# Optimization experiments

Measured on AMD Instinct MI355X. Metric: run time of the kernel, lower is better.

The kernel has to match this reference:

```python
import jax, jax.numpy as jnp
import numpy as np

# BatchNorm1d in eval mode with default init (gamma=1, beta=0, mean=0, var=1):
# y = x / sqrt(1 + eps)
BN_S = 1.0 / float(np.sqrt(1.0 + 1e-5))
ROI_THRESH = 0.8
DN = ('NCHW', 'OIHW', 'NCHW')


def conv(x, w, stride=1, pad=1):
    return jax.lax.conv_general_dilated(x, w, (stride, stride), ((pad, pad), (pad, pad)), dimension_numbers=DN)


def inv_conv(x, w):
    # dense equivalent of spconv.SparseInverseConv2d paired with a stride-2, pad-1, k=3 conv:
    # adjoint index map = transposed conv (lhs_dilation=2, flipped kernel, pad (1,2))
    return jax.lax.conv_general_dilated(x, jnp.flip(w, (2, 3)), (1, 1), ((1, 2), (1, 2)), lhs_dilation=(2, 2), dimension_numbers=DN)


def downsample_mask(m):
    # active-site generation rule of a stride-2, pad-1, k=3 sparse conv == 3x3/stride-2 max pool
    return jax.lax.reduce_window(m, 0.0, jax.lax.max, (1, 1, 3, 3), (1, 1, 2, 2), ((0, 0), (0, 0), (1, 1), (1, 1)))


def setup_inputs():
    key = jax.random.key(0)
    ks = jax.random.split(key, 24)
    b, n_i, H, W = 2, 4, 384, 384
    s = 0.1  # weight scale to keep activations bounded through the conv stack
    inp = {
        'x': jax.random.normal(ks[0], (b, 64, H // 4, W // 4), jnp.float32),
        'image': jax.random.normal(ks[1], (b, 3, H, W), jnp.float32),
        'masks': jax.random.uniform(ks[2], (b, n_i, H, W), jnp.float32),
        'roi_masks': jax.random.uniform(ks[3], (b, n_i, H, W), jnp.float32),
        'w1a': jax.random.normal(ks[4], (32, 4, 3, 3), jnp.float32) * s,
        'w1b': jax.random.normal(ks[5], (32, 32, 3, 3), jnp.float32) * s,
        'w2a': jax.random.normal(ks[6], (32, 32, 3, 3), jnp.float32) * s,
        'w2b': jax.random.normal(ks[7], (32, 32, 3, 3), jnp.float32) * s,
        'w4a': jax.random.normal(ks[8], (64, 32, 3, 3), jnp.float32) * s,
        'w4b': jax.random.normal(ks[9], (64, 64, 3, 3), jnp.float32) * s,
        'inv4_w': jax.random.normal(ks[10], (64, 64, 3, 3), jnp.float32) * s,
        'l4_sub_w': jax.random.normal(ks[11], (32, 64, 3, 3), jnp.float32) * s,
        'inv2_w': jax.random.normal(ks[12], (32, 32, 3, 3), jnp.float32) * s,
        'l5_sub_w': jax.random.normal(ks[13], (32, 32, 3, 3), jnp.float32) * s,
        'r4_w1': jax.random.normal(ks[14], (32, 64, 3, 3), jnp.float32) * s,
        'r4_w2': jax.random.normal(ks[15], (1, 32, 3, 3), jnp.float32) * s,
        'r4_b2': jax.random.normal(ks[16], (1,), jnp.float32) * s,
        'r1_w1': jax.random.normal(ks[17], (32, 32, 3, 3), jnp.float32) * s,
        'r1_w2': jax.random.normal(ks[18], (1, 32, 3, 3), jnp.float32) * s,
        'r1_b2': jax.random.normal(ks[19], (1,), jnp.float32) * s,
    }
    return inp


def reference(x, image, masks, roi_masks, w1a, w1b, w2a, w2b, w4a, w4b, inv4_w, l4_sub_w, inv2_w, l5_sub_w, r4_w1, r4_w2, r4_b2, r1_w1, r1_w2, r1_b2):
    # Faithful dense emulation of predict_details: SubMConv == conv(masked x)*mask,
    # stride-2 SparseConv == conv(masked x) masked by max-pooled mask,
    # SparseInverseConv == transposed conv masked by parent-resolution mask,
    # Fsp.sparse_add on shared indices == masked add, dense()-99/+99 == where(mask, v, -99).
    b, n_i, H, W = masks.shape
    N = b * n_i
    m = masks.reshape(N, 1, H, W)
    roi = roi_masks.reshape(N, 1, H, W)
    img = jnp.broadcast_to(image[:, None], (b, n_i, 3, H, W)).reshape(N, 3, H, W)
    inp = jnp.concatenate([img, m], axis=1)  # [N,4,H,W]

    mask1 = (roi > ROI_THRESH).astype(inp.dtype)
    mask2 = downsample_mask(mask1)
    mask4 = downsample_mask(mask2)

    # low_os1_module: SubMConv, ReLU, BN, SubMConv, ReLU, BN
    f = jnp.maximum(conv(inp * mask1, w1a) * mask1, 0.0) * BN_S
    fea1 = jnp.maximum(conv(f, w1b) * mask1, 0.0) * BN_S  # [N,32,H,W]
    # low_os2_module: stride-2 SparseConv, ReLU, BN, SubMConv, ReLU, BN
    g = jnp.maximum(conv(fea1, w2a, stride=2) * mask2, 0.0) * BN_S
    fea2 = jnp.maximum(conv(g, w2b) * mask2, 0.0) * BN_S  # [N,32,H/2,W/2]
    # low_os4_module
    h = jnp.maximum(conv(fea2, w4a, stride=2) * mask4, 0.0) * BN_S
    fea3 = jnp.maximum(conv(h, w4b) * mask4, 0.0) * BN_S  # [N,64,H/4,W/4]

    # gather dense OS4 features at sparse sites (batch index // n_i) + sparse_add
    xg = jnp.broadcast_to(x[:, None], (b, n_i) + x.shape[1:]).reshape(N, *x.shape[1:]) * mask4
    xs = xg + fea3

    # refine_OS4: SubMConv, BN, leaky, SubMConv(+bias); dense() with -99 off-support
    t = jax.nn.leaky_relu(conv(xs, r4_w1) * mask4 * BN_S, 0.2)
    t = (conv(t, r4_w2) + r4_b2[None, :, None, None]) * mask4
    x_os4_out = jnp.where(mask4 > 0, t, -99.0)

    # layer4: SparseInverseConv(64->64) to OS2 sites, BN, leaky, SubMConv(64->32); add fea2
    u = jax.nn.leaky_relu(inv_conv(xs, inv4_w) * mask2 * BN_S, 0.2)
    u = conv(u, l4_sub_w) * mask2 + fea2
    # layer5: SparseInverseConv(32->32) to OS1 sites, BN, leaky, SubMConv(32->32); add fea1
    v = jax.nn.leaky_relu(inv_conv(u, inv2_w) * mask1 * BN_S, 0.2)
    v = conv(v, l5_sub_w) * mask1 + fea1

    # refine_OS1
    t1 = jax.nn.leaky_relu(conv(v, r1_w1) * mask1 * BN_S, 0.2)
    t1 = (conv(t1, r1_w2) + r1_b2[None, :, None, None]) * mask1
    x_os1_out = jnp.where(mask1 > 0, t1, -99.0)
    return x_os4_out, x_os1_out
```

## Files before the change

### kernel.cpp

```cpp
#include <hip/hip_runtime.h>
#include <hip/hip_bf16.h>

using bf16 = __hip_bfloat16;
typedef unsigned char u8;
typedef short bf16x8 __attribute__((ext_vector_type(8)));
typedef short bf16x4 __attribute__((ext_vector_type(4)));
typedef float f32x4 __attribute__((ext_vector_type(4)));

#define BNS 0.9999950000374997f
#define MFMA_B16 __builtin_amdgcn_mfma_f32_16x16x32_bf16

__device__ __forceinline__ short f2bs(float v){ bf16 h = __float2bfloat16(v); return *reinterpret_cast<short*>(&h); }
__device__ __forceinline__ float s2f(short s){ union{unsigned u; float f;} x; x.u = ((unsigned)(unsigned short)s) << 16; return x.f; }
__device__ __forceinline__ float lrelu(float a){ return fmaxf(a, 0.2f*a); }
__device__ __forceinline__ bf16x8 ld8(const short* p){ return *(const bf16x8*)(p); }


__global__ __launch_bounds__(256) void k_mask1(const float* __restrict__ roi, u8* __restrict__ m1, int total){
    int i = blockIdx.x*256 + threadIdx.x;
    if (i < total) m1[i] = (roi[i] > 0.8f) ? 1 : 0;
}

__global__ __launch_bounds__(256) void k_down(const u8* __restrict__ mi, u8* __restrict__ mo,
                                              int IH, int IW, int OH, int OW){
    int p = blockIdx.x*256 + threadIdx.x;
    int n = blockIdx.y;
    if (p >= OH*OW) return;
    int oy = p / OW, ox = p - oy*OW;
    const u8* src = mi + (size_t)n*IH*IW;
    int v = 0;
    #pragma unroll
    for (int ky=0; ky<3; ky++){
        int iy = 2*oy + ky - 1;
        if ((unsigned)iy >= (unsigned)IH) continue;
        #pragma unroll
        for (int kx=0; kx<3; kx++){
            int ix = 2*ox + kx - 1;
            if ((unsigned)ix < (unsigned)IW) v |= src[iy*IW + ix];
        }
    }
    mo[(size_t)n*OH*OW + p] = (u8)v;
}

__global__ __launch_bounds__(256) void k_wprep(const float* __restrict__ w1b,
                                               const float* __restrict__ i2,
                                               const float* __restrict__ l5,
                                               const float* __restrict__ r1a,
                                               const float* __restrict__ w2b,
                                               const float* __restrict__ w2a,
                                               short* __restrict__ dst){
    int a = blockIdx.y;
    const float* src = (a==0)? w1b : (a==1)? i2 : (a==2)? l5 : (a==3)? r1a : (a==4)? w2b : w2a;
    float sc = (a==2) ? 1.0f : BNS;
    int j = blockIdx.x*256 + threadIdx.x;
    if (j < 9216){
        int co = j/288, r = j%288, ci = r/9, k = r%9;
        dst[a*9216 + k*1024 + co*32 + ci] = f2bs(src[j]*sc);
    }
}

__global__ __launch_bounds__(256) void k_wprep4(const float* __restrict__ inv4,
                                                const float* __restrict__ w4b,
                                                const float* __restrict__ l4s,
                                                const float* __restrict__ r4w1,
                                                const float* __restrict__ w4a,
                                                short* __restrict__ dst)
{
    int a = blockIdx.y;
    int j = blockIdx.x*256 + threadIdx.x;
    if (a < 2){
        if (j < 36864){
            int co = j/576, r = j%576, ci = r/9, k = r%9;
            const float* s = a ? w4b : inv4;
            dst[a*36864 + k*4096 + co*64 + ci] = f2bs(s[j]*BNS);
        }
    } else if (a < 4){
        if (j < 18432){
            int co = j/576, r = j%576, ci = r/9, k = r%9;
            const float* s = (a==2) ? l4s : r4w1;
            float sc = (a==2) ? 1.0f : BNS;
            dst[73728 + (a-2)*18432 + k*2048 + co*64 + ci] = f2bs(s[j]*sc);
        }
    } else {
        if (j < 18432){
            int co = j/288, r = j%288, ci = r/9, k = r%9;
            dst[110592 + k*2048 + co*32 + ci] = f2bs(w4a[j]*BNS);
        }
    }
}

__global__ __launch_bounds__(256) void k_wprep_misc(const float* __restrict__ w1a,
                                                    const float* __restrict__ r1w2,
                                                    const float* __restrict__ r4w2,
                                                    short* __restrict__ d1a,
                                                    short* __restrict__ dh){
    int a = blockIdx.y;
    int j = blockIdx.x*256 + threadIdx.x;
    if (a == 0){
        if (j < 2048){
            int h = j >> 10, r = j & 1023, co = r >> 5, kq = r & 31;
            int q = h*32 + kq;
            d1a[j] = (q < 36) ? f2bs(w1a[co*36 + q]*BNS) : 0;
        }
    } else {
        if (j < 4608){
            int k = j/512, r = j%512, co = r/32, ci = r%32;
            const float* s = (a==1) ? r1w2 : r4w2;
            dh[(a-1)*4608 + j] = (co == 0) ? f2bs(s[ci*9 + k]) : 0;
        }
    }
}

template<int CIN, int COUT, int EPI, int TH>
__global__ __launch_bounds__(256) void mconv_s1(const short* __restrict__ in, int H,
                                                const short* __restrict__ wT,
                                                const u8* __restrict__ mask,
                                                const float* __restrict__ res32,
                                                short* __restrict__ out, int tilesX)
{
    const int HW = H*H;
    const int HV = CIN/32, G = COUT/16, CH8 = CIN/8;
    const int SR = TH + 2;
    const int SITES = SR*18;
    const int PS = (SITES | 1)*8;
    const int U2N = TH/4;
    int tY = blockIdx.x / tilesX, tX = blockIdx.x % tilesX, n = blockIdx.z;
    int y0 = tY*TH, x0 = tX*16;

    __shared__ __align__(16) short s_in[CH8*((SITES|1)*8)];
    __shared__ u8 s_m[TH*16];

    int tid = threadIdx.x;
    const short* inN = in + (size_t)n*HW*CIN;
    for (int i = tid; i < SITES*CH8; i += 256){
        int r = i/CH8, q = i%CH8;
        int ry = r/18, rx = r%18;
        int gy = y0-1+ry, gx = x0-1+rx;
        bf16x8 v = {0,0,0,0,0,0,0,0};
        if ((unsigned)gy < (unsigned)H && (unsigned)gx < (unsigned)H)
            v = *(const bf16x8*)(inN + ((size_t)gy*H + gx)*CIN + q*8);
        *(bf16x8*)(s_in + q*PS + r*8) = v;
    }
    for (int i = tid; i < TH*16; i += 256){
        int ty = i>>4, tx = i&15;
        s_m[i] = mask[(size_t)n*HW + (y0+ty)*H + x0+tx];
    }
    __syncthreads();

    int wv = tid >> 6, lane = tid & 63;
    int nQ = lane >> 4, nn = lane & 15;

    f32x4 acc[U2N][G];
    #pragma unroll
    for (int u2=0; u2<U2N; ++u2)
        #pragma unroll
        for (int g=0; g<G; ++g) acc[u2][g] = (f32x4){0,0,0,0};

    #pragma unroll
    for (int h=0; h<HV; ++h){
        const short* bh[U2N];
        #pragma unroll
        for (int u2=0; u2<U2N; ++u2){
            int ty = u2*4 + wv;
            bh[u2] = s_in + (h*4+nQ)*PS + (ty*18 + nn)*8;
        }
        #pragma unroll
        for (int ky=0; ky<3; ++ky)
            #pragma unroll
            for (int kx=0; kx<3; ++kx){
                const int k = ky*3+kx;
                bf16x8 a[G];
                #pragma unroll
                for (int g=0; g<G; ++g)
                    a[g] = *(const bf16x8*)(wT + k*COUT*CIN + (g*16+nn)*CIN + h*32 + nQ*8);
                #pragma unroll
                for (int u2=0; u2<U2N; ++u2){
                    bf16x8 bfr = ld8(bh[u2] + (ky*18+kx)*8);
                    #pragma unroll
                    for (int g=0; g<G; ++g)
                        acc[u2][g] = MFMA_B16(a[g], bfr, acc[u2][g], 0,0,0);
                }
            }
    }

    #pragma unroll
    for (int u2=0; u2<U2N; ++u2){
        int nt = u2*4 + wv;
        int p = (y0+nt)*H + x0+nn;
        u8 m = s_m[nt*16 + nn];
        short* op = out + ((size_t)n*HW + p)*COUT;
        #pragma unroll
        for (int g=0; g<G; ++g){
            float r[4];
            #pragma unroll
            for (int e=0; e<4; ++e){
                int co = g*16 + nQ*4 + e;
                float a = acc[u2][g][e], o;
                if      (EPI == 0) o = m ? fmaxf(a,0.f) : 0.f;
                else if (EPI == 1) o = m ? lrelu(a) : 0.f;
                else o = m ? fmaxf(a,0.f) + res32[((size_t)(n>>2)*COUT + co)*(size_t)HW + p] : 0.f;
                r[e] = o;
            }
            bf16x4 w4 = {f2bs(r[0]),f2bs(r[1]),f2bs(r[2]),f2bs(r[3])};
            *(bf16x4*)(op + g*16 + nQ*4) = w4;
        }
    }
}

template<int TH>
__global__ __launch_bounds__(256) void mconv_head32(const short* __restrict__ in, int H,
                                                    const short* __restrict__ wTh,
                                                    const float* __restrict__ bias,
                                                    const u8* __restrict__ mask,
                                                    float* __restrict__ out, int tilesX)
{
    const int HW = H*H;
    const int SR = TH + 2, SITES = SR*18;
    const int PS = (SITES|1)*8;
    int tY = blockIdx.x / tilesX, tX = blockIdx.x % tilesX, n = blockIdx.z;
    int y0 = tY*TH, x0 = tX*16;

    __shared__ __align__(16) short s_in[4*((SITES|1)*8)];
    __shared__ u8 s_m[TH*16];

    int tid = threadIdx.x;
    const short* inN = in + (size_t)n*HW*32;
    for (int i = tid; i < SITES*4; i += 256){
        int r = i>>2, q = i&3;
        int ry = r/18, rx = r%18;
        int gy = y0-1+ry, gx = x0-1+rx;
        bf16x8 v = {0,0,0,0,0,0,0,0};
        if ((unsigned)gy < (unsigned)H && (unsigned)gx < (unsigned)H)
            v = *(const bf16x8*)(inN + ((size_t)gy*H + gx)*32 + q*8);
        *(bf16x8*)(s_in + q*PS + r*8) = v;
    }
    for (int i = tid; i < TH*16; i += 256){
        int ty = i>>4, tx = i&15;
        s_m[i] = mask[(size_t)n*HW + (y0+ty)*H + x0+tx];
    }
    __syncthreads();

    int wv = tid >> 6, lane = tid & 63;
    int nQ = lane >> 4, nn = lane & 15;
    float bb = bias[0];

    for (int nt = wv; nt < TH; nt += 4){
        const short* bp = s_in + nQ*PS + (nt*18 + nn)*8;
        f32x4 acc = {0,0,0,0};
        #pragma unroll
        for (int ky=0; ky<3; ++ky)
            #pragma unroll
            for (int kx=0; kx<3; ++kx){
                const int k = ky*3+kx;
                bf16x8 aw = *(const bf16x8*)(wTh + k*512 + nn*32 + nQ*8);
                bf16x8 bfr = ld8(bp + (ky*18+kx)*8);
                acc = MFMA_B16(aw, bfr, acc, 0,0,0);
            }
        if (nQ == 0){
            u8 m = s_m[nt*16 + nn];
            int p = (y0+nt)*H + x0+nn;
            out[(size_t)n*HW + p] = m ? acc[0] + bb : -99.f;
        }
    }
}

template<int COUT, int THO>
__global__ __launch_bounds__(256) void mconv_s2m(const short* __restrict__ in, int IH,
                                                 const short* __restrict__ wT,
                                                 const u8* __restrict__ mask,
                                                 short* __restrict__ out, int OH, int tilesX)
{
    const int IHW = IH*IH, OHW = OH*OH, G = COUT/16;
    const int IR = 2*THO + 1;
    const int SITES = IR*33;
    const int PS = (SITES|1)*8;
    const int ITN = THO/4;
    int tY = blockIdx.x / tilesX, tX = blockIdx.x % tilesX, n = blockIdx.z;
    int y0 = tY*THO, x0 = tX*16;

    __shared__ __align__(16) short s_in[4*((SITES|1)*8)];
    __shared__ u8 s_m[THO*16];

    int tid = threadIdx.x;
    const short* inN = in + (size_t)n*IHW*32;
    for (int i = tid; i < SITES*4; i += 256){
        int r = i>>2, q = i&3;
        int ry = r/33, rx = r%33;
        int gy = 2*y0-1+ry, gx = 2*x0-1+rx;
        bf16x8 v = {0,0,0,0,0,0,0,0};
        if ((unsigned)gy < (unsigned)IH && (unsigned)gx < (unsigned)IH)
            v = *(const bf16x8*)(inN + ((size_t)gy*IH + gx)*32 + q*8);
        *(bf16x8*)(s_in + q*PS + r*8) = v;
    }
    for (int i = tid; i < THO*16; i += 256){
        int ty = i>>4, tx = i&15;
        s_m[i] = mask[(size_t)n*OHW + (y0+ty)*OH + x0+tx];
    }
    __syncthreads();

    int wv = tid >> 6, lane = tid & 63;
    int nQ = lane >> 4, nn = lane & 15;

    f32x4 acc[ITN][G];
    #pragma unroll
    for (int it=0; it<ITN; ++it)
        #pragma unroll
        for (int g=0; g<G; ++g) acc[it][g] = (f32x4){0,0,0,0};

    const short* pb[ITN];
    #pragma unroll
    for (int it=0; it<ITN; ++it){
        int nt = it*4 + wv;
        pb[it] = s_in + nQ*PS + ((2*nt)*33 + 2*nn)*8;
    }

    #pragma unroll
    for (int ky=0; ky<3; ++ky)
        #pragma unroll
        for (int kx=0; kx<3; ++kx){
            const int k = ky*3+kx;
            bf16x8 a[G];
            #pragma unroll
            for (int g=0; g<G; ++g)
                a[g] = *(const bf16x8*)(wT + k*COUT*32 + (g*16+nn)*32 + nQ*8);
            #pragma unroll
            for (int it=0; it<ITN; ++it){
                bf16x8 bfr = ld8(pb[it] + (ky*33+kx)*8);
                #pragma unroll
                for (int g=0; g<G; ++g)
                    acc[it][g] = MFMA_B16(a[g], bfr, acc[it][g], 0,0,0);
            }
        }

    #pragma unroll
    for (int it=0; it<ITN; ++it){
        int nt = it*4 + wv;
        int p = (y0+nt)*OH + x0+nn;
        u8 m = s_m[nt*16 + nn];
        short* op = out + ((size_t)n*OHW + p)*COUT;
        #pragma unroll
        for (int g=0; g<G; ++g){
            float r[4];
            #pragma unroll
            for (int e=0; e<4; ++e) r[e] = m ? fmaxf(acc[it][g][e],0.f) : 0.f;
            bf16x4 w4 = {f2bs(r[0]),f2bs(r[1]),f2bs(r[2]),f2bs(r[3])};
            *(bf16x4*)(op + g*16 + nQ*4) = w4;
        }
    }
}

__global__ __launch_bounds__(256) void conv1ab3(const float* __restrict__ image,
                                                const float* __restrict__ masks,
                                                const u8*  __restrict__ M1,
                                                const short* __restrict__ wT1a,
                                                const short* __restrict__ wT1b,
                                                short* __restrict__ fea1)
{
    const int H = 384; const int HW = H*H;
    const int PS = 181*8;
    int tY = blockIdx.x / 48, tX = blockIdx.x % 48, n = blockIdx.z;
    int y0 = tY*16, x0 = tX*8;

    __shared__ float s_inp[4][240];
    __shared__ u8    s_m[240];
    __shared__ __align__(16) short s_ic[8*(181*8)];
    short* s_f = s_ic;

    int tid = threadIdx.x;
    for (int i = tid; i < 240; i += 256){
        int ly = i/12, lxx = i%12;
        int gy = y0-2+ly, gx = x0-2+lxx;
        bool inb = ((unsigned)gy < 384u) && ((unsigned)gx < 384u);
        u8 mv = inb ? M1[(size_t)n*HW + gy*H + gx] : 0;
        s_m[i] = mv;
        float mm = (float)mv;
        int p = gy*H + gx;
        #pragma unroll
        for (int c = 0; c < 4; ++c){
            float v = 0.f;
            if (inb) v = (c < 3) ? image[((size_t)(n>>2)*3 + c)*HW + p]
                                 : masks[(size_t)n*HW + p];
            s_inp[c][i] = v*mm;
        }
    }
    __syncthreads();

    for (int i = tid; i < 180*64; i += 256){
        int site = i >> 6, q = i & 63;
        short v = 0;
        if (q < 36){
            int ci = q/9, k = q - ci*9, ky = k/3, kx = k - ky*3;
            int fy = site/10, fx = site - fy*10;
            v = f2bs(s_inp[ci][(fy+ky)*12 + fx+kx]);
        }
        s_ic[(q>>3)*PS + site*8 + (q&7)] = v;
    }
    __syncthreads();

    int wv = tid >> 6, lane = tid & 63;
    int nQ = lane >> 4, nn = lane & 15;

    f32x4 fr[3][2];
    {
        #pragma unroll
        for (int u=0; u<3; ++u){ fr[u][0] = (f32x4){0,0,0,0}; fr[u][1] = (f32x4){0,0,0,0}; }
        #pragma unroll
        for (int h=0; h<2; ++h){
            bf16x8 fa0 = *(const bf16x8*)(wT1a + h*1024 + nn*32 + nQ*8);
            bf16x8 fa1 = *(const bf16x8*)(wT1a + h*1024 + (16+nn)*32 + nQ*8);
            #pragma unroll
            for (int u=0; u<3; ++u){
                int nt = u*4 + wv;
                int s0 = nt*16 + nn;
                int s = s0 > 179 ? 179 : s0;
                bf16x8 bfr = ld8(s_ic + (h*4+nQ)*PS + s*8);
                fr[u][0] = MFMA_B16(fa0, bfr, fr[u][0], 0,0,0);
                fr[u][1] = MFMA_B16(fa1, bfr, fr[u][1], 0,0,0);
            }
        }
    }
    __syncthreads();

    #pragma unroll
    for (int u=0; u<3; ++u){
        int nt = u*4 + wv;
        int s0 = nt*16 + nn;
        if (s0 <= 179){
            int fy = s0/10, fx = s0 - fy*10;
            u8 m = s_m[(fy+1)*12 + fx+1];
            #pragma unroll
            for (int g=0; g<2; ++g){
                float r[4];
                #pragma unroll
                for (int e=0; e<4; ++e){
                    float a = fr[u][g][e];
                    r[e] = m ? fmaxf(a,0.f) : 0.f;
                }
                bf16x4 w4 = {f2bs(r[0]),f2bs(r[1]),f2bs(r[2]),f2bs(r[3])};
                *(bf16x4*)(s_f + (g*2 + (nQ>>1))*PS + s0*8 + (nQ&1)*4) = w4;
            }
        }
    }
    __syncthreads();

    {
        f32x4 acc0[2], acc1[2];
        const short* pb[2];
        #pragma unroll
        for (int it=0; it<2; ++it){
            acc0[it] = (f32x4){0,0,0,0}; acc1[it] = (f32x4){0,0,0,0};
            int s0 = (it*4 + wv)*16 + nn;
            int ty = s0 >> 3, tx = s0 & 7;
            pb[it] = s_f + nQ*PS + (ty*10 + tx)*8;
        }
        #pragma unroll
        for (int ky=0; ky<3; ++ky)
            #pragma unroll
            for (int kx=0; kx<3; ++kx){
                const int k = ky*3+kx;
                bf16x8 a0 = *(const bf16x8*)(wT1b + k*1024 + nn*32 + nQ*8);
                bf16x8 a1 = *(const bf16x8*)(wT1b + k*1024 + (16+nn)*32 + nQ*8);
                #pragma unroll
                for (int it=0; it<2; ++it){
                    bf16x8 bfr = ld8(pb[it] + (ky*10+kx)*8);
                    acc0[it] = MFMA_B16(a0, bfr, acc0[it], 0,0,0);
                    acc1[it] = MFMA_B16(a1, bfr, acc1[it], 0,0,0);
                }
            }
        #pragma unroll
        for (int it=0; it<2; ++it){
            int s0 = (it*4 + wv)*16 + nn;
            int ty = s0 >> 3, tx = s0 & 7;
            u8 m = s_m[(ty+2)*12 + tx+2];
            short* fp = fea1 + ((size_t)n*HW + (size_t)(y0+ty)*H + (x0+tx))*32;
            #pragma unroll
            for (int g=0; g<2; ++g){
                float r[4];
                #pragma unroll
                for (int e=0; e<4; ++e){
                    float a = g ? acc1[it][e] : acc0[it][e];
                    r[e] = m ? fmaxf(a,0.f) : 0.f;
                }
                bf16x4 w4 = {f2bs(r[0]),f2bs(r[1]),f2bs(r[2]),f2bs(r[3])};
                *(bf16x4*)(fp + g*16 + nQ*4) = w4;
            }
        }
    }
}

__global__ __launch_bounds__(256) void fk_l4c(const short* __restrict__ xs,
                                              const short* __restrict__ fea2,
                                              const u8*  __restrict__ M2,
                                              const short* __restrict__ wTi4,
                                              const short* __restrict__ wTl4,
                                              short* __restrict__ u_out)
{
    const int H2 = 192, HW2 = H2*H2, H4 = 96, HW4 = H4*H4;
    const int PSX = 101*8, PSU = 325*8;
    int tY = blockIdx.x / 12, tX = blockIdx.x % 12, n = blockIdx.z;
    int y0 = tY*16, x0 = tX*16;
    int uy0 = (y0>>1) - 1, ux0 = (x0>>1) - 1;

    __shared__ __align__(16) short s_xs[8*(101*8)];
    __shared__ __align__(16) short s_ul[8*(325*8)];
    __shared__ u8 s_m[324];

    int tid = threadIdx.x;
    const short* xN = xs + (size_t)n*HW4*64;
    for (int i = tid; i < 100*8; i += 256){
        int r = i>>3, q = i&7;
        int ly = r/10, lxx = r%10;
        int gy = uy0+ly, gx = ux0+lxx;
        bf16x8 v = {0,0,0,0,0,0,0,0};
        if ((unsigned)gy < 96u && (unsigned)gx < 96u)
            v = *(const bf16x8*)(xN + ((size_t)gy*H4 + gx)*64 + q*8);
        *(bf16x8*)(s_xs + q*PSX + r*8) = v;
    }
    for (int i = tid; i < 324; i += 256){
        int ry = i/18, rx = i%18; int gy = y0-1+ry, gx = x0-1+rx;
        s_m[i] = ((unsigned)gy < 192u && (unsigned)gx < 192u) ? M2[(size_t)n*HW2 + gy*H2 + gx] : 0;
    }

    int wv = tid >> 6, lane = tid & 63;
    int nQ = lane >> 4, nn = lane & 15;

    bf16x4 pf2v[4][2];
    {
        const short* f2N = fea2 + (size_t)n*HW2*32;
        #pragma unroll
        for (int u2=0; u2<4; ++u2){
            int nt = u2*4 + wv;
            int p = (y0+nt)*H2 + x0+nn;
            const short* fp = f2N + (size_t)p*32;
            pf2v[u2][0] = *(const bf16x4*)(fp + nQ*4);
            pf2v[u2][1] = *(const bf16x4*)(fp + 16 + nQ*4);
        }
    }
    __syncthreads();

    for (int ui = wv; ui < 24; ui += 4){
        int cls = ui/6, nt = ui%6;
        int pY = cls >> 1, pX = cls & 1;
        int s0 = nt*16 + nn;
        int s = s0 > 80 ? 80 : s0;
        int jr = s/9, jc = s%9;
        int ry = 2*jr + pY, rx = 2*jc + pX;

        int tiy[4], tix[4], twk[4]; int tapN;
        if (pY == 0){
            if (pX == 0){
                tiy[0]=jr;   tix[0]=jc;   twk[0]=8;
                tiy[1]=jr;   tix[1]=jc+1; twk[1]=6;
                tiy[2]=jr+1; tix[2]=jc;   twk[2]=2;
                tiy[3]=jr+1; tix[3]=jc+1; twk[3]=0; tapN=4;
            } else {
                tiy[0]=jr;   tix[0]=jc+1; twk[0]=7;
                tiy[1]=jr+1; tix[1]=jc+1; twk[1]=1; tapN=2;
            }
        } else {
            if (pX == 0){
                tiy[0]=jr+1; tix[0]=jc;   twk[0]=5;
                tiy[1]=jr+1; tix[1]=jc+1; twk[1]=3; tapN=2;
            } else {
                tiy[0]=jr+1; tix[0]=jc+1; twk[0]=4; tapN=1;
            }
        }

        f32x4 acc[4];
        #pragma unroll
        for (int g=0; g<4; ++g) acc[g] = (f32x4){0,0,0,0};
        for (int t = 0; t < tapN; ++t){
            int off = (tiy[t]*10 + tix[t])*8;
            bf16x8 xlo = ld8(s_xs + nQ*PSX + off);
            bf16x8 xhi = ld8(s_xs + (4+nQ)*PSX + off);
            const short* wk = wTi4 + twk[t]*4096;
            #pragma unroll
            for (int g=0; g<4; ++g){
                bf16x8 alo = *(const bf16x8*)(wk + (g*16+nn)*64 + nQ*8);
                bf16x8 ahi = *(const bf16x8*)(wk + (g*16+nn)*64 + 32 + nQ*8);
                acc[g] = MFMA_B16(alo, xlo, acc[g], 0,0,0);
                acc[g] = MFMA_B16(ahi, xhi, acc[g], 0,0,0);
            }
        }
        if (s0 <= 80){
            int sidx = ry*18 + rx;
            u8 m = s_m[sidx];
            #pragma unroll
            for (int g=0; g<4; ++g){
                float r[4];
                #pragma unroll
                for (int e=0; e<4; ++e){
                    float a = acc[g][e];
                    r[e] = m ? lrelu(a) : 0.f;
                }
                bf16x4 w4 = {f2bs(r[0]),f2bs(r[1]),f2bs(r[2]),f2bs(r[3])};
                *(bf16x4*)(s_ul + ((g>>1)*4 + (g&1)*2 + (nQ>>1))*PSU + sidx*8 + (nQ&1)*4) = w4;
            }
        }
    }
    __syncthreads();

    {
        f32x4 acc0[4], acc1[4];
        const short* pv[4];
        #pragma unroll
        for (int u2=0; u2<4; ++u2){
            acc0[u2] = (f32x4){0,0,0,0}; acc1[u2] = (f32x4){0,0,0,0};
            int nt = u2*4 + wv;
            pv[u2] = s_ul + nQ*PSU + (nt*18 + nn)*8;
        }
        #pragma unroll
        for (int ky=0; ky<3; ++ky)
            #pragma unroll
            for (int kx=0; kx<3; ++kx){
                int k = ky*3+kx;
                const short* wk = wTl4 + k*2048;
                bf16x8 a0lo = *(const bf16x8*)(wk + nn*64 + nQ*8);
                bf16x8 a0hi = *(const bf16x8*)(wk + nn*64 + 32 + nQ*8);
                bf16x8 a1lo = *(const bf16x8*)(wk + (16+nn)*64 + nQ*8);
                bf16x8 a1hi = *(const bf16x8*)(wk + (16+nn)*64 + 32 + nQ*8);
                #pragma unroll
                for (int u2=0; u2<4; ++u2){
                    bf16x8 vlo = ld8(pv[u2] + (ky*18+kx)*8);
                    bf16x8 vhi = ld8(pv[u2] + 4*PSU + (ky*18+kx)*8);
                    acc0[u2] = MFMA_B16(a0lo, vlo, acc0[u2], 0,0,0);
                    acc0[u2] = MFMA_B16(a0hi, vhi, acc0[u2], 0,0,0);
                    acc1[u2] = MFMA_B16(a1lo, vlo, acc1[u2], 0,0,0);
                    acc1[u2] = MFMA_B16(a1hi, vhi, acc1[u2], 0,0,0);
                }
            }
        #pragma unroll
        for (int u2 = 0; u2 < 4; ++u2){
            int nt = u2*4 + wv;
            int p = (y0+nt)*H2 + x0+nn;
            u8 m = s_m[(nt+1)*18 + nn+1];
            short* up = u_out + ((size_t)n*HW2 + p)*32;
            #pragma unroll
            for (int g=0; g<2; ++g){
                float r[4];
                #pragma unroll
                for (int e=0; e<4; ++e){
                    float a = g ? acc1[u2][e] : acc0[u2][e];
                    r[e] = m ? a + s2f(pf2v[u2][g][e]) : 0.f;
                }
                bf16x4 w4 = {f2bs(r[0]),f2bs(r[1]),f2bs(r[2]),f2bs(r[3])};
                *(bf16x4*)(up + g*16 + nQ*4) = w4;
            }
        }
    }
}

__global__ __launch_bounds__(256) void fk_back8(const short* __restrict__ u,
                                                const short* __restrict__ fea1,
                                                const u8*  __restrict__ M1,
                                                const short* __restrict__ wTi2,
                                                const short* __restrict__ wTl5,
                                                const short* __restrict__ wTr1a,
                                                const short* __restrict__ wTr1b,
                                                const float* __restrict__ r1_b2,
                                                float* __restrict__ out1)
{
    const int H1 = 384, HW1 = H1*H1, H2 = 192, HW2 = H2*H2;
    const int PS_U = 97*8, PS_A = 309*8, PS_B = 241*8, PS_C = 181*8;
    int tY = blockIdx.x / 48, tX = blockIdx.x % 48, n = blockIdx.z;
    int y0 = tY*16, x0 = tX*8;
    int uy0 = (y0>>1) - 2, ux0 = (x0>>1) - 2;

    __shared__ __align__(16) short sP0[4*(309*8)];
    __shared__ __align__(16) short sP1[4*(241*8)];
    __shared__ u8 s_m[308];
    __shared__ int s_cnt[7];
    __shared__ unsigned s_lA[4*80];
    __shared__ unsigned s_lB[240];
    __shared__ unsigned s_lC[180];
    __shared__ unsigned s_lD[128];
    short* s_u  = sP1;
    short* s_vl = sP0;
    short* s_v  = sP1;
    short* s_t1 = sP0;

    int tid = threadIdx.x;
    const bf16x8 Z8 = {0,0,0,0,0,0,0,0};

    if (tid < 7) s_cnt[tid] = 0;
    const short* uN = u + (size_t)n*HW2*32;
    for (int i = tid; i < 96*4; i += 256){
        int r = i>>2, q = i&3;
        int ly = r >> 3, lxx = r & 7;
        int gy = uy0+ly, gx = ux0+lxx;
        bf16x8 v = Z8;
        if ((unsigned)gy < 192u && (unsigned)gx < 192u)
            v = *(const bf16x8*)(uN + ((size_t)gy*H2 + gx)*32 + q*8);
        *(bf16x8*)(s_u + q*PS_U + r*8) = v;
    }
    for (int i = tid; i < 308; i += 256){
        int ry = i/14, rx = i%14; int gy = y0-3+ry, gx = x0-3+rx;
        s_m[i] = ((unsigned)gy < 384u && (unsigned)gx < 384u) ? M1[(size_t)n*HW1 + gy*H1 + gx] : 0;
    }
    for (int i = tid; i < 4*309; i += 256)
        *(bf16x8*)(s_vl + i*8) = Z8;
    __syncthreads();

    for (int i = tid; i < 308; i += 256){
        if (s_m[i]){
            int ry = i/14, rx = i - ry*14;
            int cls = ((ry&1)<<1) | (rx&1);
            int jr = ry>>1, jc = rx>>1;
            int idx = atomicAdd(&s_cnt[cls], 1);
            s_lA[cls*80 + idx] = ((unsigned)i<<16) | (unsigned)(jr*8+jc);
        }
    }
    for (int i = tid; i < 240; i += 256){
        int vy = i/12, vx = i - vy*12;
        if (s_m[(vy+1)*14 + vx+1]){
            int idx = atomicAdd(&s_cnt[4], 1);
            s_lB[idx] = ((unsigned)i<<16) | (unsigned)(vy*14+vx);
        }
    }
    for (int i = tid; i < 180; i += 256){
        int qy = i/10, qx = i - qy*10;
        if (s_m[(qy+2)*14 + qx+2]){
            int idx = atomicAdd(&s_cnt[5], 1);
            s_lC[idx] = ((unsigned)i<<16) | (unsigned)(qy*12+qx);
        }
    }
    for (int i = tid; i < 128; i += 256){
        int ty = i>>3, tx = i&7;
        if (s_m[(ty+3)*14 + tx+3]){
            int idx = atomicAdd(&s_cnt[6], 1);
            s_lD[idx] = ((unsigned)i<<16) | (unsigned)(ty*10+tx);
        } else {
            out1[(size_t)n*HW1 + (size_t)(y0+ty)*H1 + (x0+tx)] = -99.f;
        }
    }
    __syncthreads();

    int wv = tid >> 6, lane = tid & 63;
    int nQ = lane >> 4, nn = lane & 15;

    {
        const int tN_[4]   = {4,2,2,1};
        const int tOff[4][4] = {{0,1,8,9},{1,9,9,9},{8,9,9,9},{9,9,9,9}};
        const int tWk [4][4] = {{8,6,2,0},{7,1,1,1},{5,3,3,3},{4,4,4,4}};
        int cnt = s_cnt[wv];
        int tn = tN_[wv];
        for (int base = 0; base < cnt; base += 16){
            int slot = base + nn;
            bool on = slot < cnt;
            unsigned e = s_lA[wv*80 + (on ? slot : 0)];
            int rb = e & 0xffff;
            f32x4 acc0 = {0,0,0,0}, acc1 = {0,0,0,0};
            for (int t = 0; t < tn; ++t){
                bf16x8 bfr = ld8(s_u + nQ*PS_U + (rb + tOff[wv][t])*8);
                const short* wp = wTi2 + tWk[wv][t]*1024;
                bf16x8 a0 = *(const bf16x8*)(wp + nn*32 + nQ*8);
                bf16x8 a1 = *(const bf16x8*)(wp + (16+nn)*32 + nQ*8);
                acc0 = MFMA_B16(a0, bfr, acc0, 0,0,0);
                acc1 = MFMA_B16(a1, bfr, acc1, 0,0,0);
            }
            if (on){
                int sidx = e >> 16;
                float r[8];
                #pragma unroll
                for (int g=0; g<2; ++g)
                    #pragma unroll
                    for (int ee=0; ee<4; ++ee)
                        r[g*4+ee] = lrelu(g ? acc1[ee] : acc0[ee]);
                bf16x4 w0 = {f2bs(r[0]),f2bs(r[1]),f2bs(r[2]),f2bs(r[3])};
                bf16x4 w1 = {f2bs(r[4]),f2bs(r[5]),f2bs(r[6]),f2bs(r[7])};
                *(bf16x4*)(s_vl + (nQ>>1)*PS_A     + sidx*8 + (nQ&1)*4) = w0;
                *(bf16x4*)(s_vl + (2+(nQ>>1))*PS_A + sidx*8 + (nQ&1)*4) = w1;
            }
        }
    }
    __syncthreads();

    for (int i = tid; i < 4*241; i += 256)
        *(bf16x8*)(s_v + i*8) = Z8;
    __syncthreads();

    {
        int cnt = s_cnt[4];
        for (int base = wv*16; base < cnt; base += 64){
            int slot = base + nn;
            bool on = slot < cnt;
            unsigned e = s_lB[on ? slot : 0];
            int rb = e & 0xffff;
            int wr = e >> 16;
            int vy = wr/12, vx = wr - vy*12;
            const short* f1 = fea1 + ((size_t)n*HW1 + (size_t)(y0-2+vy)*H1 + (x0-2+vx))*32;
            bf16x4 p0 = *(const bf16x4*)(f1 + nQ*4);
            bf16x4 p1 = *(const bf16x4*)(f1 + 16 + nQ*4);
            const short* pv = s_vl + nQ*PS_A + rb*8;
            f32x4 acc0 = {0,0,0,0}, acc1 = {0,0,0,0};
            #pragma unroll
            for (int ky=0; ky<3; ++ky)
                #pragma unroll
                for (int kx=0; kx<3; ++kx){
                    const int k = ky*3+kx;
                    bf16x8 wb0 = *(const bf16x8*)(wTl5 + k*1024 + nn*32 + nQ*8);
                    bf16x8 wb1 = *(const bf16x8*)(wTl5 + k*1024 + (16+nn)*32 + nQ*8);
                    bf16x8 bfr = ld8(pv + (ky*14+kx)*8);
                    acc0 = MFMA_B16(wb0, bfr, acc0, 0,0,0);
                    acc1 = MFMA_B16(wb1, bfr, acc1, 0,0,0);
                }
            if (on){
                float r[8];
                #pragma unroll
                for (int ee=0; ee<4; ++ee){
                    r[ee]   = acc0[ee] + s2f(p0[ee]);
                    r[4+ee] = acc1[ee] + s2f(p1[ee]);
                }
                bf16x4 w0 = {f2bs(r[0]),f2bs(r[1]),f2bs(r[2]),f2bs(r[3])};
                bf16x4 w1 = {f2bs(r[4]),f2bs(r[5]),f2bs(r[6]),f2bs(r[7])};
                *(bf16x4*)(s_v + (nQ>>1)*PS_B     + wr*8 + (nQ&1)*4) = w0;
                *(bf16x4*)(s_v + (2+(nQ>>1))*PS_B + wr*8 + (nQ&1)*4) = w1;
            }
        }
    }
    __syncthreads();

    for (int i = tid; i < 4*181; i += 256)
        *(bf16x8*)(s_t1 + i*8) = Z8;
    __syncthreads();

    {
        int cnt = s_cnt[5];
        for (int base = wv*16; base < cnt; base += 64){
            int slot = base + nn;
            bool on = slot < cnt;
            unsigned e = s_lC[on ? slot : 0];
            int rb = e & 0xffff;
            const short* pv = s_v + nQ*PS_B + rb*8;
            f32x4 acc0 = {0,0,0,0}, acc1 = {0,0,0,0};
            #pragma unroll
            for (int ky=0; ky<3; ++ky)
                #pragma unroll
                for (int kx=0; kx<3; ++kx){
                    const int k = ky*3+kx;
                    bf16x8 wc0 = *(const bf16x8*)(wTr1a + k*1024 + nn*32 + nQ*8);
                    bf16x8 wc1 = *(const bf16x8*)(wTr1a + k*1024 + (16+nn)*32 + nQ*8);
                    bf16x8 bfr = ld8(pv + (ky*12+kx)*8);
                    acc0 = MFMA_B16(wc0, bfr, acc0, 0,0,0);
                    acc1 = MFMA_B16(wc1, bfr, acc1, 0,0,0);
                }
            if (on){
                int wr = e >> 16;
                float r[8];
                #pragma unroll
                for (int g=0; g<2; ++g)
                    #pragma unroll
                    for (int ee=0; ee<4; ++ee)
                        r[g*4+ee] = lrelu(g ? acc1[ee] : acc0[ee]);
                bf16x4 w0 = {f2bs(r[0]),f2bs(r[1]),f2bs(r[2]),f2bs(r[3])};
                bf16x4 w1 = {f2bs(r[4]),f2bs(r[5]),f2bs(r[6]),f2bs(r[7])};
                *(bf16x4*)(s_t1 + (nQ>>1)*PS_C     + wr*8 + (nQ&1)*4) = w0;
                *(bf16x4*)(s_t1 + (2+(nQ>>1))*PS_C + wr*8 + (nQ&1)*4) = w1;
            }
        }
    }
    __syncthreads();

    {
        float bb = r1_b2[0];
        int cnt = s_cnt[6];
        for (int base = wv*16; base < cnt; base += 64){
            int slot = base + nn;
            bool on = slot < cnt;
            unsigned e = s_lD[on ? slot : 0];
            int rb = e & 0xffff;
            const short* pt = s_t1 + nQ*PS_C + rb*8;
            f32x4 acc = {0,0,0,0};
            #pragma unroll
            for (int ky=0; ky<3; ++ky)
                #pragma unroll
                for (int kx=0; kx<3; ++kx){
                    const int k = ky*3+kx;
                    bf16x8 aw = *(const bf16x8*)(wTr1b + k*512 + nn*32 + nQ*8);
                    bf16x8 bfr = ld8(pt + (ky*10+kx)*8);
                    acc = MFMA_B16(aw, bfr, acc, 0,0,0);
                }
            if (on && nQ == 0){
                int wr = e >> 16;
                int ty = wr >> 3, tx = wr & 7;
                out1[(size_t)n*HW1 + (size_t)(y0+ty)*H1 + (x0+tx)] = acc[0] + bb;
            }
        }
    }
}


extern "C" void kernel_launch(void* const* d_in, const int* in_sizes, int n_in,
                              void* d_out, int out_size, void* d_ws, size_t ws_size,
                              hipStream_t stream)
{
    const float* x      = (const float*)d_in[0];
    const float* image  = (const float*)d_in[1];
    const float* masks  = (const float*)d_in[2];
    const float* roi    = (const float*)d_in[3];
    const float* w1a    = (const float*)d_in[4];
    const float* w1b    = (const float*)d_in[5];
    const float* w2a    = (const float*)d_in[6];
    const float* w2b    = (const float*)d_in[7];
    const float* w4a    = (const float*)d_in[8];
    const float* w4b    = (const float*)d_in[9];
    const float* inv4_w = (const float*)d_in[10];
    const float* l4_sub = (const float*)d_in[11];
    const float* inv2_w = (const float*)d_in[12];
    const float* l5_sub = (const float*)d_in[13];
    const float* r4_w1  = (const float*)d_in[14];
    const float* r4_w2  = (const float*)d_in[15];
    const float* r4_b2  = (const float*)d_in[16];
    const float* r1_w1  = (const float*)d_in[17];
    const float* r1_w2  = (const float*)d_in[18];
    const float* r1_b2  = (const float*)d_in[19];
    float* out = (float*)d_out;

    const int N = 8;
    const int H1 = 384, HW1 = 384*384;
    const int H2 = 192, HW2 = 192*192;
    const int H4 = 96,  HW4 = 96*96;

    char* wsp = (char*)d_ws;
    size_t off = 0;
    auto alloc = [&](size_t bytes) -> char* {
        char* p = wsp + off;
        off += (bytes + 255) & ~(size_t)255;
        return p;
    };
    bf16* FEA1 = (bf16*)alloc((size_t)N*32*HW1*2);
    u8*   M1   = (u8*)alloc((size_t)N*HW1);
    u8*   M2   = (u8*)alloc((size_t)N*HW2);
    u8*   M4   = (u8*)alloc((size_t)N*HW4);
    bf16* FEA2 = (bf16*)alloc((size_t)N*32*HW2*2);
    bf16* XS   = (bf16*)alloc((size_t)N*64*HW4*2);
    bf16* GU   = (bf16*)alloc((size_t)N*32*HW2*2);
    bf16* HT   = (bf16*)alloc((size_t)N*64*HW4*2);
    short* WT   = (short*)alloc(6*9216*2);
    short* WT4  = (short*)alloc((size_t)129024*2);
    short* WT1a = (short*)alloc(2048*2);
    short* WTh  = (short*)alloc(2*4608*2);
    (void)ws_size; (void)in_sizes; (void)n_in; (void)out_size;

    short* wT1b  = WT;
    short* wTi2  = WT + 9216;
    short* wTl5  = WT + 2*9216;
    short* wTr1a = WT + 3*9216;
    short* wT2b  = WT + 4*9216;
    short* wT2a  = WT + 5*9216;
    short* wTi4  = WT4;
    short* wT4b  = WT4 + 36864;
    short* wTl4  = WT4 + 73728;
    short* wTr4a = WT4 + 92160;
    short* wT4a  = WT4 + 110592;
    short* wTr1b = WTh;
    short* wTr4b = WTh + 4608;

    dim3 blk(256);

    k_mask1<<<dim3((N*HW1 + 255)/256), blk, 0, stream>>>(roi, M1, N*HW1);
    k_down<<<dim3((HW2 + 255)/256, N), blk, 0, stream>>>(M1, M2, H1, H1, H2, H2);
    k_down<<<dim3((HW4 + 255)/256, N), blk, 0, stream>>>(M2, M4, H2, H2, H4, H4);
    k_wprep<<<dim3(36, 6), blk, 0, stream>>>(w1b, inv2_w, l5_sub, r1_w1, w2b, w2a, WT);
    k_wprep4<<<dim3(144, 5), blk, 0, stream>>>(inv4_w, w4b, l4_sub, r4_w1, w4a, WT4);
    k_wprep_misc<<<dim3(18, 3), blk, 0, stream>>>(w1a, r1_w2, r4_w2, WT1a, WTh);

    conv1ab3<<<dim3(1152, 1, N), blk, 0, stream>>>(image, masks, M1, WT1a, wT1b, (short*)FEA1);
    mconv_s2m<32,8><<<dim3(288, 1, N), blk, 0, stream>>>((const short*)FEA1, H1, wT2a, M2, (short*)GU, H2, 12);
    mconv_s1<32,32,0,8><<<dim3(288, 1, N), blk, 0, stream>>>((const short*)GU, H2, wT2b, M2, nullptr, (short*)FEA2, 12);
    mconv_s2m<64,4><<<dim3(144, 1, N), blk, 0, stream>>>((const short*)FEA2, H2, wT4a, M4, (short*)HT, H4, 6);
    mconv_s1<64,64,3,4><<<dim3(144, 1, N), blk, 0, stream>>>((const short*)HT, H4, wT4b, M4, x, (short*)XS, 6);

    mconv_s1<64,32,1,4><<<dim3(144, 1, N), blk, 0, stream>>>((const short*)XS, H4, wTr4a, M4, nullptr, (short*)HT, 6);
    mconv_head32<4><<<dim3(144, 1, N), blk, 0, stream>>>((const short*)HT, H4, wTr4b, r4_b2, M4, out, 6);

    fk_l4c<<<dim3(144, 1, N), blk, 0, stream>>>((const short*)XS, (const short*)FEA2, M2,
                                                wTi4, wTl4, (short*)GU);

    fk_back8<<<dim3(1152, 1, N), blk, 0, stream>>>((const short*)GU, (const short*)FEA1, M1,
                                                   wTi2, wTl5, wTr1a, wTr1b, r1_b2,
                                                   out + (size_t)N*HW4);
}
```

Measured before the change: 551.3 us.

## Compact active sites in conv1ab3 and run MFMA only on masked-in sites

The fused conv1a/conv1b kernel now builds per-block lists of active sites with shared atomics and runs im2col and both MFMA stages only over those sites, instead of over every site in the tile. Inactive output sites get zeros written directly. With about 20% of sites active this is meant to cut the MFMA and im2col work several-fold. In exchange it adds atomics, index indirection and a separate zero-initialised s_f buffer, which raises shared-memory use and may lower occupancy.

```diff
diff --git a/kernel.cpp b/kernel.cpp
--- a/kernel.cpp
+++ b/kernel.cpp
@@ -363,10 +363,17 @@
 
     __shared__ float s_inp[4][240];
     __shared__ u8    s_m[240];
+    __shared__ int   s_cnt[2];
+    __shared__ unsigned short s_lF[180];
+    __shared__ unsigned short s_lO[128];
     __shared__ __align__(16) short s_ic[8*(181*8)];
-    short* s_f = s_ic;
+    __shared__ __align__(16) short s_f[4*(181*8)];
 
     int tid = threadIdx.x;
+    const bf16x8 Z8 = {0,0,0,0,0,0,0,0};
+    if (tid < 2) s_cnt[tid] = 0;
+    for (int i = tid; i < 4*181; i += 256)
+        *(bf16x8*)(s_f + i*8) = Z8;
     for (int i = tid; i < 240; i += 256){
         int ly = i/12, lxx = i%12;
         int gy = y0-2+ly, gx = x0-2+lxx;
@@ -385,105 +392,117 @@
     }
     __syncthreads();
 
-    for (int i = tid; i < 180*64; i += 256){
-        int site = i >> 6, q = i & 63;
-        short v = 0;
-        if (q < 36){
-            int ci = q/9, k = q - ci*9, ky = k/3, kx = k - ky*3;
-            int fy = site/10, fx = site - fy*10;
-            v = f2bs(s_inp[ci][(fy+ky)*12 + fx+kx]);
-        }
-        s_ic[(q>>3)*PS + site*8 + (q&7)] = v;
+    for (int i = tid; i < 180; i += 256){
+        int fy = i/10, fx = i - fy*10;
+        if (s_m[(fy+1)*12 + fx+1]){
+            int idx = atomicAdd(&s_cnt[0], 1);
+            s_lF[idx] = (unsigned short)i;
+        }
+    }
+    for (int i = tid; i < 128; i += 256){
+        int ty = i>>3, tx = i&7;
+        if (s_m[(ty+2)*12 + tx+2]){
+            int idx = atomicAdd(&s_cnt[1], 1);
+            s_lO[idx] = (unsigned short)i;
+        }
+    }
+    __syncthreads();
+
+    int cntF = s_cnt[0], cntO = s_cnt[1];
+
+    {
+        int q = tid & 63;
+        int ci = q/9, kk = q - ci*9, ky = kk/3, kx = kk - ky*3;
+        bool qok = q < 36;
+        for (int i = tid; i < cntF*64; i += 256){
+            int site = s_lF[i >> 6];
+            short v = 0;
+            if (qok){
+                int fy = site/10, fx = site - fy*10;
+                v = f2bs(s_inp[ci][(fy+ky)*12 + fx+kx]);
+            }
+            s_ic[(q>>3)*PS + site*8 + (q&7)] = v;
+        }
     }
     __syncthreads();
 
     int wv = tid >> 6, lane = tid & 63;
     int nQ = lane >> 4, nn = lane & 15;
 
-    f32x4 fr[3][2];
     {
-        #pragma unroll
-        for (int u=0; u<3; ++u){ fr[u][0] = (f32x4){0,0,0,0}; fr[u][1] = (f32x4){0,0,0,0}; }
-        #pragma unroll
-        for (int h=0; h<2; ++h){
-            bf16x8 fa0 = *(const bf16x8*)(wT1a + h*1024 + nn*32 + nQ*8);
-            bf16x8 fa1 = *(const bf16x8*)(wT1a + h*1024 + (16+nn)*32 + nQ*8);
-            #pragma unroll
-            for (int u=0; u<3; ++u){
-                int nt = u*4 + wv;
-                int s0 = nt*16 + nn;
-                int s = s0 > 179 ? 179 : s0;
-                bf16x8 bfr = ld8(s_ic + (h*4+nQ)*PS + s*8);
-                fr[u][0] = MFMA_B16(fa0, bfr, fr[u][0], 0,0,0);
-                fr[u][1] = MFMA_B16(fa1, bfr, fr[u][1], 0,0,0);
-            }
-        }
-    }
-    __syncthreads();
-
-    #pragma unroll
-    for (int u=0; u<3; ++u){
-        int nt = u*4 + wv;
-        int s0 = nt*16 + nn;
-        if (s0 <= 179){
-            int fy = s0/10, fx = s0 - fy*10;
-            u8 m = s_m[(fy+1)*12 + fx+1];
-            #pragma unroll
-            for (int g=0; g<2; ++g){
-                float r[4];
-                #pragma unroll
-                for (int e=0; e<4; ++e){
-                    float a = fr[u][g][e];
-                    r[e] = m ? fmaxf(a,0.f) : 0.f;
+        bf16x8 fa0[2], fa1[2];
+        #pragma unroll
+        for (int h=0;h<2;++h){
+            fa0[h] = *(const bf16x8*)(wT1a + h*1024 + nn*32 + nQ*8);
+            fa1[h] = *(const bf16x8*)(wT1a + h*1024 + (16+nn)*32 + nQ*8);
+        }
+        for (int base = wv*16; base < cntF; base += 64){
+            int slot = base + nn;
+            bool on = slot < cntF;
+            int site = s_lF[on ? slot : 0];
+            f32x4 a0 = {0,0,0,0}, a1 = {0,0,0,0};
+            #pragma unroll
+            for (int h=0;h<2;++h){
+                bf16x8 bfr = ld8(s_ic + (h*4+nQ)*PS + site*8);
+                a0 = MFMA_B16(fa0[h], bfr, a0, 0,0,0);
+                a1 = MFMA_B16(fa1[h], bfr, a1, 0,0,0);
+            }
+            if (on){
+                #pragma unroll
+                for (int g=0; g<2; ++g){
+                    float r[4];
+                    #pragma unroll
+                    for (int e=0; e<4; ++e){
+                        float a = g ? a1[e] : a0[e];
+                        r[e] = fmaxf(a,0.f);
+                    }
+                    bf16x4 w4 = {f2bs(r[0]),f2bs(r[1]),f2bs(r[2]),f2bs(r[3])};
+                    *(bf16x4*)(s_f + (g*2 + (nQ>>1))*PS + site*8 + (nQ&1)*4) = w4;
                 }
-                bf16x4 w4 = {f2bs(r[0]),f2bs(r[1]),f2bs(r[2]),f2bs(r[3])};
-                *(bf16x4*)(s_f + (g*2 + (nQ>>1))*PS + s0*8 + (nQ&1)*4) = w4;
             }
         }
     }
     __syncthreads();
 
     {
-        f32x4 acc0[2], acc1[2];
-        const short* pb[2];
-        #pragma unroll
-        for (int it=0; it<2; ++it){
-            acc0[it] = (f32x4){0,0,0,0}; acc1[it] = (f32x4){0,0,0,0};
-            int s0 = (it*4 + wv)*16 + nn;
-            int ty = s0 >> 3, tx = s0 & 7;
-            pb[it] = s_f + nQ*PS + (ty*10 + tx)*8;
-        }
-        #pragma unroll
-        for (int ky=0; ky<3; ++ky)
-            #pragma unroll
-            for (int kx=0; kx<3; ++kx){
-                const int k = ky*3+kx;
-                bf16x8 a0 = *(const bf16x8*)(wT1b + k*1024 + nn*32 + nQ*8);
-                bf16x8 a1 = *(const bf16x8*)(wT1b + k*1024 + (16+nn)*32 + nQ*8);
-                #pragma unroll
-                for (int it=0; it<2; ++it){
-                    bf16x8 bfr = ld8(pb[it] + (ky*10+kx)*8);
-                    acc0[it] = MFMA_B16(a0, bfr, acc0[it], 0,0,0);
-                    acc1[it] = MFMA_B16(a1, bfr, acc1[it], 0,0,0);
+        for (int base = wv*16; base < cntO; base += 64){
+            int slot = base + nn;
+            bool on = slot < cntO;
+            int os = s_lO[on ? slot : 0];
+            int ty = os >> 3, tx = os & 7;
+            const short* pb = s_f + nQ*PS + (ty*10 + tx)*8;
+            f32x4 acc0 = {0,0,0,0}, acc1 = {0,0,0,0};
+            #pragma unroll
+            for (int ky=0; ky<3; ++ky)
+                #pragma unroll
+                for (int kx=0; kx<3; ++kx){
+                    const int k = ky*3+kx;
+                    bf16x8 a0 = *(const bf16x8*)(wT1b + k*1024 + nn*32 + nQ*8);
+                    bf16x8 a1 = *(const bf16x8*)(wT1b + k*1024 + (16+nn)*32 + nQ*8);
+                    bf16x8 bfr = ld8(pb + (ky*10+kx)*8);
+                    acc0 = MFMA_B16(a0, bfr, acc0, 0,0,0);
+                    acc1 = MFMA_B16(a1, bfr, acc1, 0,0,0);
                 }
-            }
-        #pragma unroll
-        for (int it=0; it<2; ++it){
-            int s0 = (it*4 + wv)*16 + nn;
-            int ty = s0 >> 3, tx = s0 & 7;
-            u8 m = s_m[(ty+2)*12 + tx+2];
-            short* fp = fea1 + ((size_t)n*HW + (size_t)(y0+ty)*H + (x0+tx))*32;
-            #pragma unroll
-            for (int g=0; g<2; ++g){
-                float r[4];
-                #pragma unroll
-                for (int e=0; e<4; ++e){
-                    float a = g ? acc1[it][e] : acc0[it][e];
-                    r[e] = m ? fmaxf(a,0.f) : 0.f;
+            if (on){
+                short* fp = fea1 + ((size_t)n*HW + (size_t)(y0+ty)*H + (x0+tx))*32;
+                #pragma unroll
+                for (int g=0; g<2; ++g){
+                    float r[4];
+                    #pragma unroll
+                    for (int e=0; e<4; ++e){
+                        float a = g ? acc1[e] : acc0[e];
+                        r[e] = fmaxf(a,0.f);
+                    }
+                    bf16x4 w4 = {f2bs(r[0]),f2bs(r[1]),f2bs(r[2]),f2bs(r[3])};
+                    *(bf16x4*)(fp + g*16 + nQ*4) = w4;
                 }
-                bf16x4 w4 = {f2bs(r[0]),f2bs(r[1]),f2bs(r[2]),f2bs(r[3])};
-                *(bf16x4*)(fp + g*16 + nQ*4) = w4;
-            }
+            }
+        }
+        for (int i = tid; i < 128*4; i += 256){
+            int os = i >> 2, q = i & 3;
+            int ty = os >> 3, tx = os & 7;
+            if (!s_m[(ty+2)*12 + tx+2])
+                *(bf16x8*)(fea1 + ((size_t)n*HW + (size_t)(y0+ty)*H + (x0+tx))*32 + q*8) = Z8;
         }
     }
 }
```

After: 528.4 us. 1.04x faster.
